# Optimization experiments

Hardware: AMD Instinct MI355X
Metric: run time of the kernel (lower is better)

## Reference

```python
import jax, jax.numpy as jnp
import numpy as np

MWH, MWW = 8, 32  # max_window_size from __init__
NUM_HEADS = 16
DIM = 512


def _relative_position_index(wh, ww):
    # static (wh, ww are python ints) -> [N, N] int index into bias table
    ch = np.arange(wh)
    cw = np.arange(ww)
    coords = np.stack(np.meshgrid(ch, cw, indexing='ij'))  # [2, wh, ww]
    cf = coords.reshape(2, -1)                              # [2, N]
    rel = cf[:, :, None] - cf[:, None, :]                   # [2, N, N]
    rel = rel.transpose(1, 2, 0).copy()                     # [N, N, 2]
    rel[:, :, 0] += MWH - 1
    rel[:, :, 1] += MWW - 1
    rel[:, :, 0] *= 2 * MWW - 1
    return jnp.asarray(rel.sum(-1))                         # [N, N]


def setup_inputs() -> dict:
    key = jax.random.key(0)
    ks = jax.random.split(key, 8)
    B_, N, C = 128, 256, DIM
    max_pos = (2 * MWH - 1) * (2 * MWW - 1)  # 945
    return {
        'x': jax.random.normal(ks[0], (B_, N, C), dtype=jnp.float32),
        'q_global': jax.random.normal(ks[1], (1, 1), dtype=jnp.float32),
        'qkv_w': jax.random.normal(ks[2], (3 * C, C), dtype=jnp.float32) * (1.0 / np.sqrt(C)),
        'qkv_b': jnp.zeros((3 * C,), dtype=jnp.float32),
        'proj_w': jax.random.normal(ks[3], (C, C), dtype=jnp.float32) * (1.0 / np.sqrt(C)),
        'proj_b': jnp.zeros((C,), dtype=jnp.float32),
        'rpb_table': jax.random.truncated_normal(ks[4], -2.0, 2.0, (max_pos, NUM_HEADS), dtype=jnp.float32) * 0.02,
        'wh': 8,
        'ww': 32,
    }


def reference(x, q_global, qkv_w, qkv_b, proj_w, proj_b, rpb_table, wh, ww):
    B_, N, C = x.shape
    H = NUM_HEADS
    hd = C // H
    scale = hd ** -0.5

    rpi = _relative_position_index(wh, ww)  # [N, N]

    qkv = x @ qkv_w.T + qkv_b                       # [B_, N, 3C]
    qkv = qkv.reshape(B_, N, 3, H, hd).transpose(2, 0, 3, 1, 4)  # [3, B_, H, N, hd]
    q, k, v = qkv[0], qkv[1], qkv[2]

    attn = jnp.einsum('bhnd,bhmd->bhnm', q * scale, k)  # [B_, H, N, N]
    bias = rpb_table[rpi.reshape(-1)].reshape(N, N, H).transpose(2, 0, 1)  # [H, N, N]
    attn = jax.nn.softmax(attn + bias[None], axis=-1)

    out = jnp.einsum('bhnm,bhmd->bhnd', attn, v)     # [B_, H, N, hd]
    out = out.transpose(0, 2, 1, 3).reshape(B_, N, C)
    return out @ proj_w.T + proj_b
```

## Files before the change

kernel.cpp:

```cpp
#include <hip/hip_runtime.h>
#include <hip/hip_fp16.h>
#include <cstdint>

typedef _Float16 f16x8 __attribute__((ext_vector_type(8)));
typedef _Float16 f16x4 __attribute__((ext_vector_type(4)));
typedef float    f32x4 __attribute__((ext_vector_type(4)));

#define MFMA16(a, b, c) __builtin_amdgcn_mfma_f32_16x16x32_f16((a), (b), (c), 0, 0, 0)

__device__ __forceinline__ void async16(_Float16* lds, const _Float16* g) {
    __builtin_amdgcn_global_load_lds(
        (const __attribute__((address_space(1))) void*)g,
        (__attribute__((address_space(3))) void*)lds, 16, 0, 0);
}

__global__ __launch_bounds__(256) void k_cvt(
    const float* __restrict__ src, _Float16* __restrict__ dst)
{
    const int i = blockIdx.x * 256 + threadIdx.x;
    const float4 a = ((const float4*)src)[2 * i];
    const float4 b = ((const float4*)src)[2 * i + 1];
    f16x8 o = { (_Float16)a.x, (_Float16)a.y, (_Float16)a.z, (_Float16)a.w,
                (_Float16)b.x, (_Float16)b.y, (_Float16)b.z, (_Float16)b.w };
    ((f16x8*)dst)[i] = o;
}

__global__ __launch_bounds__(256) void k_bias(
    const float* __restrict__ rpb, _Float16* __restrict__ bm)
{
    const int i = blockIdx.x & 255, j = threadIdx.x, h = blockIdx.x >> 8;
    const int ih = i >> 5, iw = i & 31, jh = j >> 5, jw = j & 31;
    const int idx = (ih - jh + 7) * 63 + (iw - jw + 31);
    bm[(size_t)blockIdx.x * 256 + j] = (_Float16)rpb[idx * 16 + h];
}

__global__ __launch_bounds__(256) void k_gemm_f16(
    const _Float16* __restrict__ A, int lda,
    const _Float16* __restrict__ B, int ldb,
    const float* __restrict__ bias,
    _Float16* __restrict__ C, int ldc,
    int K, int nTilesN, int cpx)
{
    __shared__ _Float16 lA[128 * 64];
    __shared__ _Float16 lB[128 * 64];
    const int t    = threadIdx.x;
    const int lane = t & 63, wv = t >> 6;
    const int fr = lane & 15, fg = lane >> 4;
    const int wrow = (wv >> 1) * 64, wcol = (wv & 1) * 64;

    const int gid  = (blockIdx.x & 7) * cpx + (blockIdx.x >> 3);
    const int row0 = (gid / nTilesN) * 128;
    const int col0 = (gid % nTilesN) * 128;

    const int rowLane = lane >> 3;
    const int colOff  = ((lane & 7) ^ rowLane) * 8;
    const int wvr = wv * 32;

    const _Float16* Ag = A + (size_t)(row0 + wvr + rowLane) * lda + colOff;
    const _Float16* Bg = B + (size_t)(col0 + wvr + rowLane) * ldb + colOff;
    _Float16* lAw = &lA[wvr * 64];
    _Float16* lBw = &lB[wvr * 64];

    f32x4 acc[4][4] = {};

    for (int k0 = 0; k0 < K; k0 += 64) {
#pragma unroll
        for (int i = 0; i < 4; ++i) {
            async16(lAw + i * 8 * 64, Ag + k0 + (size_t)i * 8 * lda);
            async16(lBw + i * 8 * 64, Bg + k0 + (size_t)i * 8 * ldb);
        }
        __syncthreads();
#pragma unroll
        for (int kk = 0; kk < 2; ++kk) {
            f16x8 af[4], bf[4];
#pragma unroll
            for (int mi = 0; mi < 4; ++mi) {
                const int ra = wrow + mi * 16 + fr;
                const int rb = wcol + mi * 16 + fr;
                const int ch = ((kk * 4 + fg) ^ (fr & 7)) * 8;
                af[mi] = *(const f16x8*)&lA[ra * 64 + ch];
                bf[mi] = *(const f16x8*)&lB[rb * 64 + ch];
            }
#pragma unroll
            for (int mi = 0; mi < 4; ++mi)
#pragma unroll
                for (int ni = 0; ni < 4; ++ni)
                    acc[mi][ni] = MFMA16(af[mi], bf[ni], acc[mi][ni]);
        }
        __syncthreads();
    }
#pragma unroll
    for (int ni = 0; ni < 4; ++ni) {
        const int col = col0 + wcol + ni * 16 + fr;
        const float bb = bias[col];
#pragma unroll
        for (int mi = 0; mi < 4; ++mi)
#pragma unroll
            for (int r = 0; r < 4; ++r) {
                const int row = row0 + wrow + mi * 16 + fg * 4 + r;
                C[(size_t)row * ldc + col] = (_Float16)(acc[mi][ni][r] + bb);
            }
    }
}

__global__ __launch_bounds__(256) void k_gemm_pf32(
    const _Float16* __restrict__ A, int lda,
    const float* __restrict__ B, int ldb,
    const float* __restrict__ bias,
    float* __restrict__ C, int ldc,
    int K, int nTilesN, int cpx)
{
    __shared__ _Float16 lA[128 * 64];
    __shared__ _Float16 lB[128 * 64];
    const int t    = threadIdx.x;
    const int lane = t & 63, wv = t >> 6;
    const int fr = lane & 15, fg = lane >> 4;
    const int wrow = (wv >> 1) * 64, wcol = (wv & 1) * 64;

    const int gid  = (blockIdx.x & 7) * cpx + (blockIdx.x >> 3);
    const int row0 = (gid / nTilesN) * 128;
    const int col0 = (gid % nTilesN) * 128;

    const int rowLane = lane >> 3;
    const int colOff  = ((lane & 7) ^ rowLane) * 8;
    const int wvr = wv * 32;

    const _Float16* Ag = A + (size_t)(row0 + wvr + rowLane) * lda + colOff;
    _Float16* lAw = &lA[wvr * 64];

    const int sb = t >> 1, cb = (t & 1) * 32;
    const float* Bg = B + (size_t)(col0 + sb) * ldb + cb;

    f32x4 acc[4][4] = {};

    for (int k0 = 0; k0 < K; k0 += 64) {
#pragma unroll
        for (int i = 0; i < 4; ++i)
            async16(lAw + i * 8 * 64, Ag + k0 + (size_t)i * 8 * lda);
#pragma unroll
        for (int c = 0; c < 4; ++c) {
            float4 u = *(const float4*)(Bg + k0 + c * 8);
            float4 v = *(const float4*)(Bg + k0 + c * 8 + 4);
            f16x8 hv = { (_Float16)u.x, (_Float16)u.y, (_Float16)u.z, (_Float16)u.w,
                         (_Float16)v.x, (_Float16)v.y, (_Float16)v.z, (_Float16)v.w };
            const int ch = (cb >> 3) + c;
            *(f16x8*)&lB[sb * 64 + ((ch ^ (sb & 7)) * 8)] = hv;
        }
        __syncthreads();
#pragma unroll
        for (int kk = 0; kk < 2; ++kk) {
            f16x8 af[4], bf[4];
#pragma unroll
            for (int mi = 0; mi < 4; ++mi) {
                const int ra = wrow + mi * 16 + fr;
                const int rb = wcol + mi * 16 + fr;
                const int ch = ((kk * 4 + fg) ^ (fr & 7)) * 8;
                af[mi] = *(const f16x8*)&lA[ra * 64 + ch];
                bf[mi] = *(const f16x8*)&lB[rb * 64 + ch];
            }
#pragma unroll
            for (int mi = 0; mi < 4; ++mi)
#pragma unroll
                for (int ni = 0; ni < 4; ++ni)
                    acc[mi][ni] = MFMA16(af[mi], bf[ni], acc[mi][ni]);
        }
        __syncthreads();
    }
#pragma unroll
    for (int ni = 0; ni < 4; ++ni) {
        const int col = col0 + wcol + ni * 16 + fr;
        const float bb = bias[col];
#pragma unroll
        for (int mi = 0; mi < 4; ++mi)
#pragma unroll
            for (int r = 0; r < 4; ++r) {
                const int row = row0 + wrow + mi * 16 + fg * 4 + r;
                C[(size_t)row * ldc + col] = acc[mi][ni][r] + bb;
            }
    }
}

#define ATT_SCALE 0.17677669529663687f

__global__ __launch_bounds__(256) void k_attn(
    _Float16* __restrict__ qkv, const _Float16* __restrict__ bm)
{
    __shared__ _Float16 lS[4][16 * 264];
    __shared__ _Float16 lVt[32 * 264];

    const int bh = blockIdx.x;
    const int b = bh >> 4, h = bh & 15;
    const int t = threadIdx.x, wv = t >> 6, lane = t & 63;
    const int fr = lane & 15, fg = lane >> 4;

    _Float16* qkv_b0 = qkv + (size_t)b * 256 * 1536;
    const _Float16* bias_h = bm + (size_t)h * 256 * 256;

    {
        const _Float16* vrow = qkv_b0 + (size_t)t * 1536 + 1024 + h * 32;
        f16x8 v0 = *(const f16x8*)(vrow);
        f16x8 v1 = *(const f16x8*)(vrow + 8);
        f16x8 v2 = *(const f16x8*)(vrow + 16);
        f16x8 v3 = *(const f16x8*)(vrow + 24);
#pragma unroll
        for (int d = 0; d < 8; ++d) {
            lVt[(d     ) * 264 + t] = v0[d];
            lVt[(d +  8) * 264 + t] = v1[d];
            lVt[(d + 16) * 264 + t] = v2[d];
            lVt[(d + 24) * 264 + t] = v3[d];
        }
    }
    __syncthreads();

    _Float16* myS = &lS[wv][0];

    for (int rb = 0; rb < 4; ++rb) {
        const int r0 = wv * 64 + rb * 16;

        f16x8 aq = *(const f16x8*)(qkv_b0 + (size_t)(r0 + fr) * 1536 + h * 32 + fg * 8);

#pragma unroll 4
        for (int jt = 0; jt < 16; ++jt) {
            f16x8 bk = *(const f16x8*)(qkv_b0 + (size_t)(jt * 16 + fr) * 1536 + 512 + h * 32 + fg * 8);
            f32x4 s = { 0.f, 0.f, 0.f, 0.f };
            s = MFMA16(aq, bk, s);
#pragma unroll
            for (int r = 0; r < 4; ++r)
                myS[(fg * 4 + r) * 264 + jt * 16 + fr] = (_Float16)(s[r] * ATT_SCALE);
        }

        f16x8 tb[8];
        {
            const _Float16* brow = bias_h + (size_t)(r0 + fr) * 256 + fg * 8;
#pragma unroll
            for (int kc = 0; kc < 8; ++kc)
                tb[kc] = *(const f16x8*)(brow + kc * 32);
        }
        asm volatile("s_waitcnt lgkmcnt(0)" ::: "memory");

        float vmax = -1e30f;
#pragma unroll
        for (int kc = 0; kc < 8; ++kc) {
            f16x8 sv = *(const f16x8*)(&myS[fr * 264 + kc * 32 + fg * 8]);
            tb[kc] = tb[kc] + sv;
#pragma unroll
            for (int j = 0; j < 8; ++j)
                vmax = fmaxf(vmax, (float)tb[kc][j]);
        }
        vmax = fmaxf(vmax, __shfl_xor(vmax, 16));
        vmax = fmaxf(vmax, __shfl_xor(vmax, 32));

        float rsum = 0.f;
#pragma unroll
        for (int kc = 0; kc < 8; ++kc) {
#pragma unroll
            for (int j = 0; j < 8; ++j) {
                float p = __expf((float)tb[kc][j] - vmax);
                rsum += p;
                tb[kc][j] = (_Float16)p;
            }
        }
        rsum += __shfl_xor(rsum, 16);
        rsum += __shfl_xor(rsum, 32);

        f32x4 o[2] = {};
#pragma unroll
        for (int kc = 0; kc < 8; ++kc) {
            f16x8 bv0 = *(const f16x8*)(&lVt[(fr     ) * 264 + kc * 32 + fg * 8]);
            f16x8 bv1 = *(const f16x8*)(&lVt[(fr + 16) * 264 + kc * 32 + fg * 8]);
            o[0] = MFMA16(tb[kc], bv0, o[0]);
            o[1] = MFMA16(tb[kc], bv1, o[1]);
        }
        float os[4];
#pragma unroll
        for (int r = 0; r < 4; ++r) os[r] = __shfl(rsum, fg * 4 + r);

#pragma unroll
        for (int ni = 0; ni < 2; ++ni)
#pragma unroll
            for (int r = 0; r < 4; ++r) {
                const int i = r0 + fg * 4 + r;
                const int d = ni * 16 + fr;
                qkv_b0[(size_t)i * 1536 + h * 32 + d] = (_Float16)(o[ni][r] / os[r]);
            }
    }
}

extern "C" void kernel_launch(void* const* d_in, const int* in_sizes, int n_in,
                              void* d_out, int out_size, void* d_ws, size_t ws_size,
                              hipStream_t stream)
{
    (void)in_sizes; (void)n_in;
    const float* x      = (const float*)d_in[0];
    const float* qkv_w  = (const float*)d_in[2];
    const float* qkv_b  = (const float*)d_in[3];
    const float* proj_w = (const float*)d_in[4];
    const float* proj_b = (const float*)d_in[5];
    const float* rpb    = (const float*)d_in[6];
    float* out = (float*)d_out;

    const int M  = 128 * 256;
    const int Cd = 512, N3 = 1536;

    const size_t need = (size_t)M * N3 * sizeof(_Float16);
    if (ws_size < need) {
        (void)hipMemsetAsync(d_out, 0, (size_t)out_size * sizeof(float), stream);
        return;
    }

    _Float16* qkvh = (_Float16*)d_ws;
    _Float16* xh   = (_Float16*)d_out;
    _Float16* qwh  = xh + (size_t)M * Cd;
    _Float16* bmat = qwh + (size_t)N3 * Cd;

    k_cvt<<<dim3((M * Cd) / 2048), 256, 0, stream>>>(x, xh);
    k_cvt<<<dim3((N3 * Cd) / 2048), 256, 0, stream>>>(qkv_w, qwh);
    k_bias<<<dim3(16 * 256), 256, 0, stream>>>(rpb, bmat);

    k_gemm_f16<<<dim3(3072), 256, 0, stream>>>(xh, Cd, qwh, Cd, qkv_b,
                                               qkvh, N3, Cd, 12, 384);
    k_attn<<<dim3(128 * 16), 256, 0, stream>>>(qkvh, bmat);
    k_gemm_pf32<<<dim3(1024), 256, 0, stream>>>(qkvh, N3, proj_w, Cd, proj_b,
                                                out, Cd, Cd, 4, 128);
}
```

Before: 371.0 us.

## Store Q/K/V in head-major [H,B,N,hd] layout across GEMM, attention, projection

The QKV GEMM epilogue now scatters results into three separate head-major buffers of shape [H,B,N,32] instead of a packed [M,1536] row. Attention then reads contiguous 64-byte rows per token for Q, K and V rather than strided 3KB rows. The projection GEMM gathers its A operand from this head-major layout. This aims to make attention loads contiguous, at the cost of more scattered epilogue stores and gather loads in the projection.

```diff
diff --git a/kernel.cpp b/kernel.cpp
--- a/kernel.cpp
+++ b/kernel.cpp
@@ -34,11 +34,12 @@
     bm[(size_t)blockIdx.x * 256 + j] = (_Float16)rpb[idx * 16 + h];
 }
 
-__global__ __launch_bounds__(256) void k_gemm_f16(
+__global__ __launch_bounds__(256) void k_gemm_qkv(
     const _Float16* __restrict__ A, int lda,
-    const _Float16* __restrict__ B, int ldb,
+    const _Float16* __restrict__ Bm, int ldb,
     const float* __restrict__ bias,
-    _Float16* __restrict__ C, int ldc,
+    _Float16* __restrict__ Qh, _Float16* __restrict__ Kh,
+    _Float16* __restrict__ Vh,
     int K, int nTilesN, int cpx)
 {
     __shared__ _Float16 lA[128 * 64];
@@ -57,7 +58,7 @@
     const int wvr = wv * 32;
 
     const _Float16* Ag = A + (size_t)(row0 + wvr + rowLane) * lda + colOff;
-    const _Float16* Bg = B + (size_t)(col0 + wvr + rowLane) * ldb + colOff;
+    const _Float16* Bg = Bm + (size_t)(col0 + wvr + rowLane) * ldb + colOff;
     _Float16* lAw = &lA[wvr * 64];
     _Float16* lBw = &lB[wvr * 64];
 
@@ -89,22 +90,30 @@
         }
         __syncthreads();
     }
+
+    const int b  = row0 >> 8;
+    const int nb = row0 & 255;
 #pragma unroll
     for (int ni = 0; ni < 4; ++ni) {
-        const int col = col0 + wcol + ni * 16 + fr;
-        const float bb = bias[col];
+        const int colb  = col0 + wcol + ni * 16;
+        const int which = colb >> 9;
+        const int h     = (colb >> 5) & 15;
+        const int d0    = colb & 31;
+        _Float16* T = which == 0 ? Qh : (which == 1 ? Kh : Vh);
+        _Float16* p = T + (size_t)(h * 128 + b) * 8192 + d0 + fr;
+        const float bb = bias[colb + fr];
 #pragma unroll
         for (int mi = 0; mi < 4; ++mi)
 #pragma unroll
             for (int r = 0; r < 4; ++r) {
-                const int row = row0 + wrow + mi * 16 + fg * 4 + r;
-                C[(size_t)row * ldc + col] = (_Float16)(acc[mi][ni][r] + bb);
-            }
-    }
-}
-
-__global__ __launch_bounds__(256) void k_gemm_pf32(
-    const _Float16* __restrict__ A, int lda,
+                const int n = nb + wrow + mi * 16 + fg * 4 + r;
+                p[(size_t)n * 32] = (_Float16)(acc[mi][ni][r] + bb);
+            }
+    }
+}
+
+__global__ __launch_bounds__(256) void k_proj(
+    const _Float16* __restrict__ Qh,
     const float* __restrict__ B, int ldb,
     const float* __restrict__ bias,
     float* __restrict__ C, int ldc,
@@ -125,7 +134,8 @@
     const int colOff  = ((lane & 7) ^ rowLane) * 8;
     const int wvr = wv * 32;
 
-    const _Float16* Ag = A + (size_t)(row0 + wvr + rowLane) * lda + colOff;
+    const int bidx = row0 >> 8;
+    const int nb   = (row0 & 255) + wvr + rowLane;
     _Float16* lAw = &lA[wvr * 64];
 
     const int sb = t >> 1, cb = (t & 1) * 32;
@@ -134,9 +144,12 @@
     f32x4 acc[4][4] = {};
 
     for (int k0 = 0; k0 < K; k0 += 64) {
+        const int kc = k0 + colOff;
+        const int hh = kc >> 5, dd = kc & 31;
+        const _Float16* src = Qh + (size_t)(hh * 128 + bidx) * 8192 + dd;
 #pragma unroll
         for (int i = 0; i < 4; ++i)
-            async16(lAw + i * 8 * 64, Ag + k0 + (size_t)i * 8 * lda);
+            async16(lAw + i * 8 * 64, src + (size_t)(nb + i * 8) * 32);
 #pragma unroll
         for (int c = 0; c < 4; ++c) {
             float4 u = *(const float4*)(Bg + k0 + c * 8);
@@ -183,7 +196,8 @@
 #define ATT_SCALE 0.17677669529663687f
 
 __global__ __launch_bounds__(256) void k_attn(
-    _Float16* __restrict__ qkv, const _Float16* __restrict__ bm)
+    _Float16* __restrict__ Qh, const _Float16* __restrict__ Kh,
+    const _Float16* __restrict__ Vh, const _Float16* __restrict__ bm)
 {
     __shared__ _Float16 lS[4][16 * 264];
     __shared__ _Float16 lVt[32 * 264];
@@ -193,11 +207,14 @@
     const int t = threadIdx.x, wv = t >> 6, lane = t & 63;
     const int fr = lane & 15, fg = lane >> 4;
 
-    _Float16* qkv_b0 = qkv + (size_t)b * 256 * 1536;
+    const size_t base = (size_t)(h * 128 + b) * 8192;
+    _Float16* qb = Qh + base;
+    const _Float16* kb = Kh + base;
+    const _Float16* vb = Vh + base;
     const _Float16* bias_h = bm + (size_t)h * 256 * 256;
 
     {
-        const _Float16* vrow = qkv_b0 + (size_t)t * 1536 + 1024 + h * 32;
+        const _Float16* vrow = vb + (size_t)t * 32;
         f16x8 v0 = *(const f16x8*)(vrow);
         f16x8 v1 = *(const f16x8*)(vrow + 8);
         f16x8 v2 = *(const f16x8*)(vrow + 16);
@@ -217,11 +234,11 @@
     for (int rb = 0; rb < 4; ++rb) {
         const int r0 = wv * 64 + rb * 16;
 
-        f16x8 aq = *(const f16x8*)(qkv_b0 + (size_t)(r0 + fr) * 1536 + h * 32 + fg * 8);
+        f16x8 aq = *(const f16x8*)(qb + (size_t)(r0 + fr) * 32 + fg * 8);
 
 #pragma unroll 4
         for (int jt = 0; jt < 16; ++jt) {
-            f16x8 bk = *(const f16x8*)(qkv_b0 + (size_t)(jt * 16 + fr) * 1536 + 512 + h * 32 + fg * 8);
+            f16x8 bk = *(const f16x8*)(kb + (size_t)(jt * 16 + fr) * 32 + fg * 8);
             f32x4 s = { 0.f, 0.f, 0.f, 0.f };
             s = MFMA16(aq, bk, s);
 #pragma unroll
@@ -280,8 +297,7 @@
 #pragma unroll
             for (int r = 0; r < 4; ++r) {
                 const int i = r0 + fg * 4 + r;
-                const int d = ni * 16 + fr;
-                qkv_b0[(size_t)i * 1536 + h * 32 + d] = (_Float16)(o[ni][r] / os[r]);
+                qb[(size_t)i * 32 + ni * 16 + fr] = (_Float16)(o[ni][r] / os[r]);
             }
     }
 }
@@ -301,14 +317,17 @@
 
     const int M  = 128 * 256;
     const int Cd = 512, N3 = 1536;
-
-    const size_t need = (size_t)M * N3 * sizeof(_Float16);
+    const size_t HBN = (size_t)16 * 128 * 256 * 32;
+
+    const size_t need = 3 * HBN * sizeof(_Float16);
     if (ws_size < need) {
         (void)hipMemsetAsync(d_out, 0, (size_t)out_size * sizeof(float), stream);
         return;
     }
 
-    _Float16* qkvh = (_Float16*)d_ws;
+    _Float16* Qh = (_Float16*)d_ws;
+    _Float16* Kh = Qh + HBN;
+    _Float16* Vh = Kh + HBN;
     _Float16* xh   = (_Float16*)d_out;
     _Float16* qwh  = xh + (size_t)M * Cd;
     _Float16* bmat = qwh + (size_t)N3 * Cd;
@@ -317,9 +336,9 @@
     k_cvt<<<dim3((N3 * Cd) / 2048), 256, 0, stream>>>(qkv_w, qwh);
     k_bias<<<dim3(16 * 256), 256, 0, stream>>>(rpb, bmat);
 
-    k_gemm_f16<<<dim3(3072), 256, 0, stream>>>(xh, Cd, qwh, Cd, qkv_b,
-                                               qkvh, N3, Cd, 12, 384);
-    k_attn<<<dim3(128 * 16), 256, 0, stream>>>(qkvh, bmat);
-    k_gemm_pf32<<<dim3(1024), 256, 0, stream>>>(qkvh, N3, proj_w, Cd, proj_b,
-                                                out, Cd, Cd, 4, 128);
-}
+    k_gemm_qkv<<<dim3(3072), 256, 0, stream>>>(xh, Cd, qwh, Cd, qkv_b,
+                                               Qh, Kh, Vh, Cd, 12, 384);
+    k_attn<<<dim3(128 * 16), 256, 0, stream>>>(Qh, Kh, Vh, bmat);
+    k_proj<<<dim3(1024), 256, 0, stream>>>(Qh, proj_w, Cd, proj_b,
+                                           out, Cd, Cd, 4, 128);
+}
```

Measured after the change: 347.4 us. 1.07x faster.
